# Kernel optimization log

Measured on AMD Instinct MI355X. Metric: run time of the kernel, lower is better.

The kernel has to match this reference:

```python
import jax, jax.numpy as jnp
import numpy as np

B, N, D = 1, 4096, 512
H, HD = 8, 64
NBINS = 512
CAND = 64
SCALE = 1.0 / np.sqrt(HD)
MAX_NORM = 1.0 - 1e-5
TWO_PI = 2.0 * np.pi


def _project(x):
    # Poincare-ball style projection: clip L2 norm of each point to MAX_NORM.
    n = jnp.sqrt(jnp.sum(x * x, axis=-1, keepdims=True))
    s = jnp.minimum(1.0, MAX_NORM / jnp.maximum(n, 1e-12))
    return x * s


def _bins(x):
    # Deterministic geometric binning (DavisCache stand-in): quantize the
    # angle of the first two coordinates into NBINS bins.
    ang = jnp.arctan2(x[..., 1], x[..., 0])  # (-pi, pi]
    b = jnp.floor((ang / TWO_PI + 0.5) * NBINS)
    return jnp.clip(b, 0, NBINS - 1).astype(jnp.int32)


def setup_inputs() -> dict:
    key0 = jax.random.key(0)
    ks = jax.random.split(key0, 12)
    w = 0.02  # typical init scale for projection weights
    return {
        "query": jax.random.normal(ks[0], (B, N, D), dtype=jnp.float32),
        "key": jax.random.normal(ks[1], (B, N, D), dtype=jnp.float32),
        "value": jax.random.normal(ks[2], (B, N, D), dtype=jnp.float32),
        "Wq": jax.random.normal(ks[3], (D, D), dtype=jnp.float32) * w,
        "bq": jnp.zeros((D,), dtype=jnp.float32),
        "Wk": jax.random.normal(ks[4], (D, D), dtype=jnp.float32) * w,
        "bk": jnp.zeros((D,), dtype=jnp.float32),
        "Wv": jax.random.normal(ks[5], (D, D), dtype=jnp.float32) * w,
        "bv": jnp.zeros((D,), dtype=jnp.float32),
        "Wo": jax.random.normal(ks[6], (D, D), dtype=jnp.float32) * w,
        "bo": jnp.zeros((D,), dtype=jnp.float32),
    }


def reference(query, key, value, Wq, bq, Wk, bk, Wv, bv, Wo, bo):
    Bq, Nq, Dm = query.shape
    Nk = key.shape[1]
    # projections + split heads -> (B, H, N, HD)
    q = (query @ Wq.T + bq).reshape(Bq, Nq, H, HD).transpose(0, 2, 1, 3)
    k = (key @ Wk.T + bk).reshape(Bq, Nk, H, HD).transpose(0, 2, 1, 3)
    v = (value @ Wv.T + bv).reshape(Bq, Nk, H, HD).transpose(0, 2, 1, 3)
    q = _project(q)
    k = _project(k)

    # geometric binning; candidate keys for a query are those whose bin is
    # within radius 1 of the query's bin (neighboring_bins, radius=1).
    qb = _bins(q)  # (B, H, Nq) int32
    kb = _bins(k)  # (B, H, Nk) int32
    mask = jnp.abs(qb[..., :, None] - kb[..., None, :]) <= 1  # (B,H,Nq,Nk)
    # fallback: if a query has no candidates, attend over all keys
    any_valid = jnp.any(mask, axis=-1, keepdims=True)
    eff = jnp.where(any_valid, mask, True)
    # keep only the first CAND candidates per query (by key index)
    rank = jnp.cumsum(eff.astype(jnp.int32), axis=-1) - 1
    sel = eff & (rank < CAND)

    scores = jnp.einsum("bhqd,bhkd->bhqk", q, k) * SCALE
    scores = jnp.where(sel, scores, -jnp.inf)
    attn = jax.nn.softmax(scores, axis=-1)  # dropout p=0.0 (eval mode)
    out = jnp.einsum("bhqk,bhkd->bhqd", attn, v)

    out = out.transpose(0, 2, 1, 3).reshape(Bq, Nq, Dm)
    return out @ Wo.T + bo
```

## Files before the change

kernel.cpp:

```cpp
#include <hip/hip_runtime.h>
#include <math.h>

typedef unsigned short u16;
typedef __attribute__((ext_vector_type(8))) short v8bf;
typedef __attribute__((ext_vector_type(4))) float f32x4;

#define N_TOK 4096
#define DMODEL 512
#define NHEAD 8
#define HDIM 64
#define CANDN 64
#define NBINS 512
#define BINCAP 64
#define QCAP 128
#define ATT_SCALE 0.125f
#define MAX_NORM_F 0.99999f

__device__ __forceinline__ float bf2f(u16 u) {
  union { unsigned int i; float f; } v; v.i = ((unsigned int)u) << 16; return v.f;
}
__device__ __forceinline__ u16 f2bf(float f) {
  union { float f; unsigned int i; } v; v.f = f;
  unsigned int x = v.i;
  return (u16)((x + 0x7fffu + ((x >> 16) & 1u)) >> 16);
}
__device__ __forceinline__ uint4 load_pack8(const float* __restrict__ p) {
  const float4 x0 = *(const float4*)p;
  const float4 x1 = *(const float4*)(p + 4);
  union { u16 h[8]; uint4 u; } r;
  r.h[0] = f2bf(x0.x); r.h[1] = f2bf(x0.y); r.h[2] = f2bf(x0.z); r.h[3] = f2bf(x0.w);
  r.h[4] = f2bf(x1.x); r.h[5] = f2bf(x1.y); r.h[6] = f2bf(x1.z); r.h[7] = f2bf(x1.w);
  return r.u;
}

__global__ __launch_bounds__(256) void prep_kernel(
    const float* __restrict__ query, const float* __restrict__ key_,
    const float* __restrict__ value,
    const float* __restrict__ Wq, const float* __restrict__ Wk,
    const float* __restrict__ Wv, const float* __restrict__ Wo,
    u16* __restrict__ qx, u16* __restrict__ kx, u16* __restrict__ vx,
    u16* __restrict__ wqx, u16* __restrict__ wkx, u16* __restrict__ wvx,
    u16* __restrict__ wox,
    int* __restrict__ qb, int* __restrict__ kb, unsigned char* __restrict__ flags,
    int* __restrict__ khist)
{
  __shared__ float xs[16 * 516];
  const int blk = blockIdx.x;
  const int tid = threadIdx.x;

  if (blk >= 4096) {
    int4 z4; z4.x = 0; z4.y = 0; z4.z = 0; z4.w = 0;
    ((int4*)khist)[((blk - 4096) << 8) + tid] = z4;
    return;
  }

  if (blk >= 512) {
    const int rel = blk - 512;
    const float* src; u16* dst; int base;
    if (rel < 1024)      { src = query; dst = qx; base = rel << 11; }
    else if (rel < 2048) { src = key_;  dst = kx; base = (rel - 1024) << 11; }
    else if (rel < 3072) { src = value; dst = vx; base = (rel - 2048) << 11; }
    else {
      const int r2 = rel - 3072; const int w = r2 >> 7;
      src = (w == 0) ? Wq : (w == 1) ? Wk : (w == 2) ? Wv : Wo;
      dst = (w == 0) ? wqx : (w == 1) ? wkx : (w == 2) ? wvx : wox;
      base = (r2 & 127) << 11;
    }
    const int off = base + tid * 8;
    *(uint4*)(dst + off) = load_pack8(src + off);
    return;
  }

  const int isk  = blk >> 8;
  const int tile = blk & 255;
  const float* X = isk ? key_ : query;
  const float* W = isk ? Wk : Wq;

#pragma unroll
  for (int i = 0; i < 8; ++i) {
    const int flat = i * 1024 + tid * 4;
    const int row = flat >> 9, col = flat & 511;
    *(float4*)&xs[row * 516 + col] = *(const float4*)(X + (tile * 16 + row) * DMODEL + col);
  }
  __syncthreads();

  const int n_local = tid >> 4;
  const int pair = tid & 15;
  const int h = pair >> 1, coord = pair & 1;
  const float* wrow = W + ((h << 6) + coord) * DMODEL;
  const float* xrow = &xs[n_local * 516];

  double c0 = 0.0, c1 = 0.0, c2 = 0.0, c3 = 0.0;
  for (int k = 0; k < DMODEL; k += 4) {
    const float4 xv = *(const float4*)(xrow + k);
    const float4 wv = *(const float4*)(wrow + k);
    c0 = fma((double)xv.x, (double)wv.x, c0);
    c1 = fma((double)xv.y, (double)wv.y, c1);
    c2 = fma((double)xv.z, (double)wv.z, c2);
    c3 = fma((double)xv.w, (double)wv.w, c3);
  }
  const double a = (c0 + c1) + (c2 + c3);
  const double other = __shfl_xor(a, 1);
  if (coord == 0) {
    const double a0 = a, a1 = other;
    const int n = tile * 16 + n_local;
    double ang = atan2(a1, a0);
    double t = (ang / 6.283185307179586 + 0.5) * 512.0;
    int b = (int)floor(t);
    b = b < 0 ? 0 : (b > 511 ? 511 : b);
    (isk ? kb : qb)[(h << 12) + n] = b;

    const double r = sqrt(a0 * a0 + a1 * a1);
    const double dist = fabs(t - nearbyint(t));
    const double margin = fmin(0.45, 3.3e-4 / fmax(r, 1e-30) + 5e-5);
    flags[(isk << 15) | (h << 12) | n] = (dist < margin) ? 1 : 0;
  }
}

__device__ float fdlibm_atanf(float x) {
#pragma clang fp contract(off)
  const float atanhi[4] = {4.6364760399e-01f, 7.8539812565e-01f,
                           9.8279368877e-01f, 1.5707962513e+00f};
  const float atanlo[4] = {5.0121582440e-09f, 3.7748947079e-08f,
                           3.4473217170e-08f, 7.5497894159e-08f};
  const float aT[5] = {3.3333328366e-01f, -1.9999158382e-01f, 1.4253635705e-01f,
                       -1.0648017377e-01f, 6.1687607318e-02f};
  unsigned ix = __float_as_uint(x);
  const unsigned sign = ix >> 31;
  ix &= 0x7fffffffu;
  int id;
  float z, w, s1, s2;
  if (ix >= 0x4c800000u) {
    z = atanhi[3] + 0x1p-120f;
    return sign ? -z : z;
  }
  if (ix < 0x3ee00000u) {
    if (ix < 0x39800000u) return x;
    id = -1;
  } else {
    x = fabsf(x);
    if (ix < 0x3f980000u) {
      if (ix < 0x3f300000u) { id = 0; x = (2.0f * x - 1.0f) / (2.0f + x); }
      else                  { id = 1; x = (x - 1.0f) / (x + 1.0f); }
    } else {
      if (ix < 0x401c0000u) { id = 2; x = (x - 1.5f) / (1.0f + 1.5f * x); }
      else                  { id = 3; x = -1.0f / x; }
    }
  }
  z = x * x;
  w = z * z;
  s1 = z * (aT[0] + w * (aT[2] + w * aT[4]));
  s2 = w * (aT[1] + w * aT[3]);
  if (id < 0) return x - x * (s1 + s2);
  z = atanhi[id] - ((x * (s1 + s2) - atanlo[id]) - x);
  return sign ? -z : z;
}

__device__ float fdlibm_atan2f(float y, float x) {
#pragma clang fp contract(off)
  const float pi = 3.1415927410e+00f, pi_lo = -8.7422776573e-08f;
  const unsigned hx = __float_as_uint(x), hy = __float_as_uint(y);
  if (hx == 0x3f800000u) return fdlibm_atanf(y);
  const unsigned m = ((hy >> 31) & 1u) | ((hx >> 30) & 2u);
  const unsigned ix = hx & 0x7fffffffu, iy = hy & 0x7fffffffu;
  if (iy == 0u) {
    switch (m) { case 0: case 1: return y; case 2: return pi; default: return -pi; }
  }
  if (ix == 0u) return (m & 1u) ? -1.57079637050628662f : 1.57079637050628662f;
  float z;
  if (ix + (26u << 23) < iy) {
    z = 1.57079637050628662f;
    return (m & 1u) ? -z : z;
  }
  if ((m & 2u) && iy + (26u << 23) < ix) z = 0.0f;
  else z = fdlibm_atanf(fabsf(y / x));
  switch (m) {
    case 0: return z;
    case 1: return -z;
    case 2: return pi - (z - pi_lo);
    default: return (z - pi_lo) - pi;
  }
}

__global__ __launch_bounds__(256) void gemmfix_kernel(
    const u16* __restrict__ qx, const u16* __restrict__ kx, const u16* __restrict__ vx,
    const u16* __restrict__ wqx, const u16* __restrict__ wkx, const u16* __restrict__ wvx,
    const float* __restrict__ bq, const float* __restrict__ bk, const float* __restrict__ bv,
    const float* __restrict__ query, const float* __restrict__ key_,
    const float* __restrict__ Wq, const float* __restrict__ Wk,
    const unsigned char* __restrict__ flags,
    int* __restrict__ qb, int* __restrict__ kb,
    u16* __restrict__ Qb, u16* __restrict__ Kb, u16* __restrict__ Vb)
{
  __shared__ u16 As[2][128 * 40];
  __shared__ u16 Ws[2][128 * 40];
  __shared__ int wle[64];
  __shared__ int wlc;

  const int blk = blockIdx.x;
  const int tid = threadIdx.x;

  if (blk >= 384) {
    const int slice = blk - 384;
    if (tid == 0) wlc = 0;
    __syncthreads();
    for (int i = tid; i < 1024; i += 256) {
      const int flat = slice * 1024 + i;
      if (flags[flat]) {
        const int p = atomicAdd(&wlc, 1);
        if (p < 64) wle[p] = flat;
      }
    }
    __syncthreads();
    int nw = wlc; if (nw > 64) nw = 64;
    const int w = tid >> 6, d = tid & 63;
    for (int e = w; e < nw; e += 4) {
      const int flat = wle[e];
      const int n = flat & 4095;
      const int h = (flat >> 12) & 7;
      const int isk = flat >> 15;
      const float* xr = (isk ? key_ : query) + n * DMODEL;
      const float* wr = (isk ? Wk : Wq) + ((h << 6) + d) * DMODEL;
      float acc = 0.0f;
      for (int k = 0; k < DMODEL; k += 16) {
        const float4 xa = *(const float4*)(xr + k);
        const float4 xb = *(const float4*)(xr + k + 4);
        const float4 xc = *(const float4*)(xr + k + 8);
        const float4 xd = *(const float4*)(xr + k + 12);
        const float4 wa = *(const float4*)(wr + k);
        const float4 wb = *(const float4*)(wr + k + 4);
        const float4 wc = *(const float4*)(wr + k + 8);
        const float4 wd = *(const float4*)(wr + k + 12);
        acc = __fmaf_rn(xa.x, wa.x, acc); acc = __fmaf_rn(xa.y, wa.y, acc);
        acc = __fmaf_rn(xa.z, wa.z, acc); acc = __fmaf_rn(xa.w, wa.w, acc);
        acc = __fmaf_rn(xb.x, wb.x, acc); acc = __fmaf_rn(xb.y, wb.y, acc);
        acc = __fmaf_rn(xb.z, wb.z, acc); acc = __fmaf_rn(xb.w, wb.w, acc);
        acc = __fmaf_rn(xc.x, wc.x, acc); acc = __fmaf_rn(xc.y, wc.y, acc);
        acc = __fmaf_rn(xc.z, wc.z, acc); acc = __fmaf_rn(xc.w, wc.w, acc);
        acc = __fmaf_rn(xd.x, wd.x, acc); acc = __fmaf_rn(xd.y, wd.y, acc);
        acc = __fmaf_rn(xd.z, wd.z, acc); acc = __fmaf_rn(xd.w, wd.w, acc);
      }
      {
#pragma clang fp contract(off)
        const float sq = acc * acc;
        float rr[8];
#pragma unroll
        for (int j = 0; j < 8; ++j) rr[j] = __shfl(sq, j);
        for (int i = 8; i < 64; i += 8) {
#pragma unroll
          for (int j = 0; j < 8; ++j) rr[j] += __shfl(sq, i + j);
        }
        const float ss = ((rr[0] + rr[1]) + (rr[2] + rr[3])) +
                         ((rr[4] + rr[5]) + (rr[6] + rr[7]));
        const float nrm = __fsqrt_rn(ss);
        const float s = fminf(1.0f, 0.99999f / fmaxf(nrm, 1e-12f));
        const float c0 = __shfl(acc, 0) * s;
        const float c1 = __shfl(acc, 1) * s;
        const float cr = (float)atan2((double)c1, (double)c0);
        const float fd = fdlibm_atan2f(c1, c0);
        const float tol = fmaxf(fabsf(cr) * 6e-7f, 1e-30f);
        const float ang = (fabsf(fd - cr) <= tol) ? fd : cr;
        const float t = ((ang / 6.2831854820251465f) + 0.5f) * 512.0f;
        int b = (int)floorf(t);
        b = b < 0 ? 0 : (b > 511 ? 511 : b);
        if (d == 0) (isk ? kb : qb)[(h << 12) + n] = b;
      }
    }
    return;
  }

  const int z = blk >> 7;
  const int rem = blk & 127;
  const int bm = (rem & 31) * 128;
  const int bn = (rem >> 5) * 128;

  const u16* A    = (z == 0) ? qx : (z == 1) ? kx : vx;
  const u16* W    = (z == 0) ? wqx : (z == 1) ? wkx : wvx;
  const float* bias = (z == 0) ? bq : (z == 1) ? bk : bv;
  u16* O          = (z == 0) ? Qb : (z == 1) ? Kb : Vb;

  const int lane = tid & 63;
  const int wave = tid >> 6;
  const int row4 = tid >> 2;
  const int seg  = tid & 3;
  const int wm = (wave & 1) * 64;
  const int wn = (wave >> 1) * 64;
  const int l15 = lane & 15;
  const int quad = lane >> 4;

  f32x4 acc[4][4] = {};

  uint4 a0 = *(const uint4*)(A + (bm + row4) * DMODEL + seg * 8);
  uint4 a1 = *(const uint4*)(A + (bm + row4 + 64) * DMODEL + seg * 8);
  uint4 w0 = *(const uint4*)(W + (bn + row4) * DMODEL + seg * 8);
  uint4 w1 = *(const uint4*)(W + (bn + row4 + 64) * DMODEL + seg * 8);

  for (int kt = 0; kt < DMODEL; kt += 32) {
    const int p = (kt >> 5) & 1;
    *(uint4*)&As[p][row4 * 40 + seg * 8] = a0;
    *(uint4*)&As[p][(row4 + 64) * 40 + seg * 8] = a1;
    *(uint4*)&Ws[p][row4 * 40 + seg * 8] = w0;
    *(uint4*)&Ws[p][(row4 + 64) * 40 + seg * 8] = w1;
    __syncthreads();
    if (kt + 32 < DMODEL) {
      a0 = *(const uint4*)(A + (bm + row4) * DMODEL + kt + 32 + seg * 8);
      a1 = *(const uint4*)(A + (bm + row4 + 64) * DMODEL + kt + 32 + seg * 8);
      w0 = *(const uint4*)(W + (bn + row4) * DMODEL + kt + 32 + seg * 8);
      w1 = *(const uint4*)(W + (bn + row4 + 64) * DMODEL + kt + 32 + seg * 8);
    }
    v8bf af[4], bfr[4];
#pragma unroll
    for (int i = 0; i < 4; ++i)
      af[i] = *(const v8bf*)&As[p][(wm + i * 16 + l15) * 40 + quad * 8];
#pragma unroll
    for (int j = 0; j < 4; ++j)
      bfr[j] = *(const v8bf*)&Ws[p][(wn + j * 16 + l15) * 40 + quad * 8];
#pragma unroll
    for (int i = 0; i < 4; ++i)
#pragma unroll
      for (int j = 0; j < 4; ++j)
        acc[i][j] = __builtin_amdgcn_mfma_f32_16x16x32_bf16(af[i], bfr[j], acc[i][j], 0, 0, 0);
  }

  float bval[4];
#pragma unroll
  for (int j = 0; j < 4; ++j) bval[j] = bias[bn + wn + j * 16 + l15];
  const int h = (bn + wn) >> 6;

#pragma unroll
  for (int i = 0; i < 4; ++i) {
#pragma unroll
    for (int r = 0; r < 4; ++r) {
      const int row = bm + wm + i * 16 + quad * 4 + r;
      float v0 = acc[i][0][r] + bval[0];
      float v1 = acc[i][1][r] + bval[1];
      float v2 = acc[i][2][r] + bval[2];
      float v3 = acc[i][3][r] + bval[3];
      if (z != 2) {
        float ss = v0 * v0 + v1 * v1 + v2 * v2 + v3 * v3;
#pragma unroll
        for (int o = 1; o < 16; o <<= 1) ss += __shfl_xor(ss, o);
        const float s = fminf(1.0f, MAX_NORM_F / fmaxf(sqrtf(ss), 1e-12f));
        v0 *= s; v1 *= s; v2 *= s; v3 *= s;
      }
      const int base = (((h << 12) + row) << 6) + l15;
      O[base +  0] = f2bf(v0); O[base + 16] = f2bf(v1);
      O[base + 32] = f2bf(v2); O[base + 48] = f2bf(v3);
    }
  }
}

__global__ __launch_bounds__(256) void bin_hist_kernel(
    const int* __restrict__ kb, const int* __restrict__ qb,
    int* __restrict__ khist, u16* __restrict__ blist,
    int* __restrict__ qhist, u16* __restrict__ qlist)
{
  const int h = blockIdx.x;
  const int type = blockIdx.y;
  const int* src = type ? qb : kb;
  int* hist = type ? qhist : khist;
  u16* list = type ? qlist : blist;
  const int cap = type ? QCAP : BINCAP;

  const int i = blockIdx.z * 256 + threadIdx.x;
  const int b = src[(h << 12) + i];
  const int pos = atomicAdd(&hist[(h << 9) + b], 1);
  if (pos < cap) list[((h << 9) + b) * cap + pos] = (u16)i;
}

__global__ __launch_bounds__(64) void attn_bin_kernel(
    const u16* __restrict__ Qb, const u16* __restrict__ Kb,
    const u16* __restrict__ Vb, const int* __restrict__ qhist,
    const u16* __restrict__ qlist, const int* __restrict__ khist,
    const u16* __restrict__ blist, u16* __restrict__ aout)
{
  __shared__ u16 kf[4 * 2 * 4 * 16 * 8];
  __shared__ u16 vf[4 * 2 * 4 * 16 * 8];
  __shared__ u16 pf[16 * 72];
  __shared__ u16 s_cand[64];
  __shared__ int s_qg[16];

  const int hb = blockIdx.x;
  const int h = hb >> 9;
  const int b = hb & 511;
  int qcnt = qhist[hb];
  if (qcnt > QCAP) qcnt = QCAP;
  if (qcnt == 0) return;

  const int lane = threadIdx.x;
  const int l15 = lane & 15;
  const int quad = lane >> 4;

  int v0 = 0xFFFF, v1 = 0xFFFF, v2 = 0xFFFF;
  int c0 = 0, c1 = 0, c2 = 0;
  if (b > 0) {
    c0 = khist[(h << 9) + b - 1];
    if (c0 > BINCAP) c0 = BINCAP;
    if (lane < c0) v0 = (int)blist[(((h << 9) + b - 1) << 6) + lane];
  }
  {
    c1 = khist[(h << 9) + b];
    if (c1 > BINCAP) c1 = BINCAP;
    if (lane < c1) v1 = (int)blist[(((h << 9) + b) << 6) + lane];
  }
  if (b < NBINS - 1) {
    c2 = khist[(h << 9) + b + 1];
    if (c2 > BINCAP) c2 = BINCAP;
    if (lane < c2) v2 = (int)blist[(((h << 9) + b + 1) << 6) + lane];
  }

  int r0 = 0, r1 = 0, r2 = 0;
#pragma unroll 8
  for (int j = 0; j < 64; ++j) {
    const int w0 = __shfl(v0, j);
    const int w1 = __shfl(v1, j);
    const int w2 = __shfl(v2, j);
    r0 += (w0 < v0) + (w1 < v0) + (w2 < v0);
    r1 += (w0 < v1) + (w1 < v1) + (w2 < v1);
    r2 += (w0 < v2) + (w1 < v2) + (w2 < v2);
  }
  const int tot = c0 + c1 + c2;
  const int ccnt = tot < CANDN ? tot : CANDN;
  const int ccnt_eff = (tot == 0) ? 64 : ccnt;
  if (tot == 0) {
    s_cand[lane] = (u16)lane;
  } else {
    if (v0 != 0xFFFF && r0 < CANDN) s_cand[r0] = (u16)v0;
    if (v1 != 0xFFFF && r1 < CANDN) s_cand[r1] = (u16)v1;
    if (v2 != 0xFFFF && r2 < CANDN) s_cand[r2] = (u16)v2;
  }
  __syncthreads();
  if (tot > 0 && lane >= ccnt) s_cand[lane] = s_cand[0];
  __syncthreads();

  {
    const int r = lane >> 3, s = lane & 7;
    const int ks = s >> 2, qd = s & 3;
#pragma unroll
    for (int it = 0; it < 8; ++it) {
      const int key = it * 8 + r;
      const int c = s_cand[key];
      const uint4 kv = *(const uint4*)(Kb + ((h << 18) | (c << 6)) + s * 8);
      const int idx = ((((key >> 4) * 2 + ks) * 4 + qd) * 16 + (key & 15)) * 8;
      *(uint4*)&kf[idx] = kv;
    }
  }
  {
    const int r = lane >> 3, s = lane & 7;
    const int nt = s >> 1, d0 = (s & 1) * 8;
#pragma unroll
    for (int it = 0; it < 8; ++it) {
      const int key = it * 8 + r;
      const int c = s_cand[key];
      union { u16 hh[8]; uint4 u; } vv;
      vv.u = *(const uint4*)(Vb + ((h << 18) | (c << 6)) + s * 8);
      const int kstep = key >> 5, qd = (key >> 3) & 3, j = key & 7;
#pragma unroll
      for (int m = 0; m < 8; ++m)
        vf[(((nt * 2 + kstep) * 4 + qd) * 16 + d0 + m) * 8 + j] = vv.hh[m];
    }
  }
  __syncthreads();

  v8bf akf[4][2], bvf[4][2];
#pragma unroll
  for (int t = 0; t < 4; ++t)
#pragma unroll
    for (int ks = 0; ks < 2; ++ks) {
      akf[t][ks] = *(const v8bf*)&kf[(((t * 2 + ks) * 4 + quad) * 16 + l15) * 8];
      bvf[t][ks] = *(const v8bf*)&vf[(((t * 2 + ks) * 4 + quad) * 16 + l15) * 8];
    }

  const int nchunk = (qcnt + 15) >> 4;
  for (int ci = 0; ci < nchunk; ++ci) {
    const int base = ci << 4;
    const int qcn = min(16, qcnt - base);
    __syncthreads();
    if (lane < 16) {
      int idx = base + lane;
      if (idx > qcnt - 1) idx = qcnt - 1;
      s_qg[lane] = (int)qlist[(hb << 7) + idx];
    }
    __syncthreads();

    const u16* qrow = Qb + ((h << 18) | (s_qg[l15] << 6));
    v8bf bq[2];
#pragma unroll
    for (int ks = 0; ks < 2; ++ks)
      bq[ks] = *(const v8bf*)(qrow + ks * 32 + quad * 8);

    float sc[16];
    __builtin_amdgcn_s_setprio(1);
#pragma unroll
    for (int t = 0; t < 4; ++t) {
      f32x4 sa = {0.f, 0.f, 0.f, 0.f};
      sa = __builtin_amdgcn_mfma_f32_16x16x32_bf16(akf[t][0], bq[0], sa, 0, 0, 0);
      sa = __builtin_amdgcn_mfma_f32_16x16x32_bf16(akf[t][1], bq[1], sa, 0, 0, 0);
#pragma unroll
      for (int r = 0; r < 4; ++r) {
        const int key = t * 16 + quad * 4 + r;
        sc[t * 4 + r] = (key < ccnt_eff) ? sa[r] * ATT_SCALE : -INFINITY;
      }
    }
    __builtin_amdgcn_s_setprio(0);
    float mx = sc[0];
#pragma unroll
    for (int i = 1; i < 16; ++i) mx = fmaxf(mx, sc[i]);
    mx = fmaxf(mx, __shfl_xor(mx, 16));
    mx = fmaxf(mx, __shfl_xor(mx, 32));
    float sum = 0.0f;
    float pe[16];
#pragma unroll
    for (int i = 0; i < 16; ++i) { pe[i] = __expf(sc[i] - mx); sum += pe[i]; }
    sum += __shfl_xor(sum, 16);
    sum += __shfl_xor(sum, 32);
    const float inv = 1.0f / sum;

    __syncthreads();
#pragma unroll
    for (int t = 0; t < 4; ++t)
#pragma unroll
      for (int r = 0; r < 4; ++r)
        pf[l15 * 72 + t * 16 + quad * 4 + r] = f2bf(pe[t * 4 + r] * inv);
    __syncthreads();

    v8bf ap[2];
#pragma unroll
    for (int ks = 0; ks < 2; ++ks)
      ap[ks] = *(const v8bf*)&pf[l15 * 72 + ks * 32 + quad * 8];

    __builtin_amdgcn_s_setprio(1);
#pragma unroll
    for (int nt = 0; nt < 4; ++nt) {
      f32x4 o = {0.f, 0.f, 0.f, 0.f};
      o = __builtin_amdgcn_mfma_f32_16x16x32_bf16(ap[0], bvf[nt][0], o, 0, 0, 0);
      o = __builtin_amdgcn_mfma_f32_16x16x32_bf16(ap[1], bvf[nt][1], o, 0, 0, 0);
#pragma unroll
      for (int r = 0; r < 4; ++r) {
        const int row = quad * 4 + r;
        if (row < qcn)
          aout[s_qg[row] * DMODEL + (h << 6) + nt * 16 + l15] = f2bf(o[r]);
      }
    }
    __builtin_amdgcn_s_setprio(0);
  }
}

__global__ __launch_bounds__(256) void gemm_out_kernel(
    const u16* __restrict__ A, const u16* __restrict__ W,
    const float* __restrict__ bias, float* __restrict__ O)
{
  __shared__ u16 As[2][128 * 40];
  __shared__ u16 Ws[2][128 * 40];

  const int tid  = threadIdx.x;
  const int lane = tid & 63;
  const int wave = tid >> 6;
  const int row4 = tid >> 2;
  const int seg  = tid & 3;

  const int bm = blockIdx.x * 128;
  const int bn = blockIdx.y * 128;
  const int wm = (wave & 1) * 64;
  const int wn = (wave >> 1) * 64;
  const int l15 = lane & 15;
  const int quad = lane >> 4;

  f32x4 acc[4][4] = {};

  uint4 a0 = *(const uint4*)(A + (bm + row4) * DMODEL + seg * 8);
  uint4 a1 = *(const uint4*)(A + (bm + row4 + 64) * DMODEL + seg * 8);
  uint4 w0 = *(const uint4*)(W + (bn + row4) * DMODEL + seg * 8);
  uint4 w1 = *(const uint4*)(W + (bn + row4 + 64) * DMODEL + seg * 8);

  for (int kt = 0; kt < DMODEL; kt += 32) {
    const int p = (kt >> 5) & 1;
    *(uint4*)&As[p][row4 * 40 + seg * 8] = a0;
    *(uint4*)&As[p][(row4 + 64) * 40 + seg * 8] = a1;
    *(uint4*)&Ws[p][row4 * 40 + seg * 8] = w0;
    *(uint4*)&Ws[p][(row4 + 64) * 40 + seg * 8] = w1;
    __syncthreads();
    if (kt + 32 < DMODEL) {
      a0 = *(const uint4*)(A + (bm + row4) * DMODEL + kt + 32 + seg * 8);
      a1 = *(const uint4*)(A + (bm + row4 + 64) * DMODEL + kt + 32 + seg * 8);
      w0 = *(const uint4*)(W + (bn + row4) * DMODEL + kt + 32 + seg * 8);
      w1 = *(const uint4*)(W + (bn + row4 + 64) * DMODEL + kt + 32 + seg * 8);
    }
    v8bf af[4], bfr[4];
#pragma unroll
    for (int i = 0; i < 4; ++i)
      af[i] = *(const v8bf*)&As[p][(wm + i * 16 + l15) * 40 + quad * 8];
#pragma unroll
    for (int j = 0; j < 4; ++j)
      bfr[j] = *(const v8bf*)&Ws[p][(wn + j * 16 + l15) * 40 + quad * 8];
#pragma unroll
    for (int i = 0; i < 4; ++i)
#pragma unroll
      for (int j = 0; j < 4; ++j)
        acc[i][j] = __builtin_amdgcn_mfma_f32_16x16x32_bf16(af[i], bfr[j], acc[i][j], 0, 0, 0);
  }

#pragma unroll
  for (int j = 0; j < 4; ++j) {
    const int cg = bn + wn + j * 16 + l15;
    const float bval = bias[cg];
#pragma unroll
    for (int i = 0; i < 4; ++i) {
      const int rbase = bm + wm + i * 16 + quad * 4;
#pragma unroll
      for (int r = 0; r < 4; ++r)
        O[(rbase + r) * DMODEL + cg] = acc[i][j][r] + bval;
    }
  }
}

extern "C" void kernel_launch(void* const* d_in, const int* in_sizes, int n_in,
                              void* d_out, int out_size, void* d_ws, size_t ws_size,
                              hipStream_t stream) {
  const float* query = (const float*)d_in[0];
  const float* key_  = (const float*)d_in[1];
  const float* value = (const float*)d_in[2];
  const float* Wq = (const float*)d_in[3];
  const float* bq = (const float*)d_in[4];
  const float* Wk = (const float*)d_in[5];
  const float* bk = (const float*)d_in[6];
  const float* Wv = (const float*)d_in[7];
  const float* bv = (const float*)d_in[8];
  const float* Wo = (const float*)d_in[9];
  const float* bo = (const float*)d_in[10];

  char* ws = (char*)d_ws;
  u16* qx    = (u16*)(ws);
  u16* kx    = (u16*)(ws + 4194304);
  u16* vx    = (u16*)(ws + 8388608);
  u16* wqx   = (u16*)(ws + 12582912);
  u16* wkx   = (u16*)(ws + 13107200);
  u16* wvx   = (u16*)(ws + 13631488);
  u16* wox   = (u16*)(ws + 14155776);
  u16* Qb    = (u16*)(ws + 14680064);
  u16* Kb    = (u16*)(ws + 18874368);
  u16* Vb    = (u16*)(ws + 23068672);
  u16* aout  = (u16*)(ws + 27262976);
  int* qb    = (int*)(ws + 31457280);
  int* kb    = (int*)(ws + 31588352);
  unsigned char* flags = (unsigned char*)(ws + 31719424);
  int* khist = (int*)(ws + 31784960);
  int* qhist = (int*)(ws + 31801344);
  u16* blist = (u16*)(ws + 31817728);
  u16* qlist = (u16*)(ws + 32342016);

  prep_kernel<<<4104, 256, 0, stream>>>(
      query, key_, value, Wq, Wk, Wv, Wo,
      qx, kx, vx, wqx, wkx, wvx, wox, qb, kb, flags, khist);
  gemmfix_kernel<<<448, 256, 0, stream>>>(
      qx, kx, vx, wqx, wkx, wvx, bq, bk, bv,
      query, key_, Wq, Wk, flags, qb, kb, Qb, Kb, Vb);
  bin_hist_kernel<<<dim3(8, 2, 16), 256, 0, stream>>>(
      kb, qb, khist, blist, qhist, qlist);
  attn_bin_kernel<<<4096, 64, 0, stream>>>(
      Qb, Kb, Vb, qhist, qlist, khist, blist, aout);
  gemm_out_kernel<<<dim3(32, 4), 256, 0, stream>>>(aout, wox, bo, (float*)d_out);
}
```

Baseline: 213.1 us.

## Split bin-fix into own kernel, grid-stride prep conversion, halve output GEMM M-tile

The prep kernel's conversion and histogram-zeroing blocks become one grid-stride loop over fewer blocks. The fp32 bin-fix work moves out of the QKV GEMM kernel into a separate kernel with 512 smaller slices, so the fix work no longer tails behind the GEMM blocks. The output GEMM tile shrinks from 128 to 64 rows, doubling its grid to fill more CUs. This adds one more kernel launch and lowers per-block reuse in the output GEMM.

After: 200.3 us. 6.0% less time.

```diff
diff --git a/kernel.cpp b/kernel.cpp
--- a/kernel.cpp
+++ b/kernel.cpp
@@ -48,26 +48,27 @@
   const int blk = blockIdx.x;
   const int tid = threadIdx.x;
 
-  if (blk >= 4096) {
-    int4 z4; z4.x = 0; z4.y = 0; z4.z = 0; z4.w = 0;
-    ((int4*)khist)[((blk - 4096) << 8) + tid] = z4;
-    return;
-  }
-
   if (blk >= 512) {
-    const int rel = blk - 512;
-    const float* src; u16* dst; int base;
-    if (rel < 1024)      { src = query; dst = qx; base = rel << 11; }
-    else if (rel < 2048) { src = key_;  dst = kx; base = (rel - 1024) << 11; }
-    else if (rel < 3072) { src = value; dst = vx; base = (rel - 2048) << 11; }
-    else {
-      const int r2 = rel - 3072; const int w = r2 >> 7;
-      src = (w == 0) ? Wq : (w == 1) ? Wk : (w == 2) ? Wv : Wo;
-      dst = (w == 0) ? wqx : (w == 1) ? wkx : (w == 2) ? wvx : wox;
-      base = (r2 & 127) << 11;
-    }
-    const int off = base + tid * 8;
-    *(uint4*)(dst + off) = load_pack8(src + off);
+    const int base = ((blk - 512) << 8) + tid;
+    for (int u = base; u < 919552; u += 262144) {
+      if (u < 786432) {
+        const int third = u >> 18;
+        const int off = (u & 262143) << 3;
+        const float* src = (third == 0) ? query : (third == 1) ? key_ : value;
+        u16* dst = (third == 0) ? qx : (third == 1) ? kx : vx;
+        *(uint4*)(dst + off) = load_pack8(src + off);
+      } else if (u < 917504) {
+        const int r2 = u - 786432;
+        const int w = r2 >> 15;
+        const int off = (r2 & 32767) << 3;
+        const float* src = (w == 0) ? Wq : (w == 1) ? Wk : (w == 2) ? Wv : Wo;
+        u16* dst = (w == 0) ? wqx : (w == 1) ? wkx : (w == 2) ? wvx : wox;
+        *(uint4*)(dst + off) = load_pack8(src + off);
+      } else {
+        int4 z4; z4.x = 0; z4.y = 0; z4.z = 0; z4.w = 0;
+        ((int4*)khist)[u - 917504] = z4;
+      }
+    }
     return;
   }
 
@@ -182,92 +183,95 @@
   }
 }
 
-__global__ __launch_bounds__(256) void gemmfix_kernel(
+__global__ __launch_bounds__(256) void binfix_kernel(
+    const float* __restrict__ query, const float* __restrict__ key_,
+    const float* __restrict__ Wq, const float* __restrict__ Wk,
+    const unsigned char* __restrict__ flags,
+    int* __restrict__ qb, int* __restrict__ kb)
+{
+  __shared__ int wle[64];
+  __shared__ int wlc;
+
+  const int tid = threadIdx.x;
+  const int slice = blockIdx.x;
+
+  if (tid == 0) wlc = 0;
+  __syncthreads();
+  if (tid < 128) {
+    const int flat = (slice << 7) + tid;
+    if (flags[flat]) {
+      const int p = atomicAdd(&wlc, 1);
+      if (p < 64) wle[p] = flat;
+    }
+  }
+  __syncthreads();
+  int nw = wlc; if (nw > 64) nw = 64;
+  const int w = tid >> 6, d = tid & 63;
+  for (int e = w; e < nw; e += 4) {
+    const int flat = wle[e];
+    const int n = flat & 4095;
+    const int h = (flat >> 12) & 7;
+    const int isk = flat >> 15;
+    const float* xr = (isk ? key_ : query) + n * DMODEL;
+    const float* wr = (isk ? Wk : Wq) + ((h << 6) + d) * DMODEL;
+    float acc = 0.0f;
+    for (int k = 0; k < DMODEL; k += 16) {
+      const float4 xa = *(const float4*)(xr + k);
+      const float4 xb = *(const float4*)(xr + k + 4);
+      const float4 xc = *(const float4*)(xr + k + 8);
+      const float4 xd = *(const float4*)(xr + k + 12);
+      const float4 wa = *(const float4*)(wr + k);
+      const float4 wb = *(const float4*)(wr + k + 4);
+      const float4 wc = *(const float4*)(wr + k + 8);
+      const float4 wd = *(const float4*)(wr + k + 12);
+      acc = __fmaf_rn(xa.x, wa.x, acc); acc = __fmaf_rn(xa.y, wa.y, acc);
+      acc = __fmaf_rn(xa.z, wa.z, acc); acc = __fmaf_rn(xa.w, wa.w, acc);
+      acc = __fmaf_rn(xb.x, wb.x, acc); acc = __fmaf_rn(xb.y, wb.y, acc);
+      acc = __fmaf_rn(xb.z, wb.z, acc); acc = __fmaf_rn(xb.w, wb.w, acc);
+      acc = __fmaf_rn(xc.x, wc.x, acc); acc = __fmaf_rn(xc.y, wc.y, acc);
+      acc = __fmaf_rn(xc.z, wc.z, acc); acc = __fmaf_rn(xc.w, wc.w, acc);
+      acc = __fmaf_rn(xd.x, wd.x, acc); acc = __fmaf_rn(xd.y, wd.y, acc);
+      acc = __fmaf_rn(xd.z, wd.z, acc); acc = __fmaf_rn(xd.w, wd.w, acc);
+    }
+    {
+#pragma clang fp contract(off)
+      const float sq = acc * acc;
+      float rr[8];
+#pragma unroll
+      for (int j = 0; j < 8; ++j) rr[j] = __shfl(sq, j);
+      for (int i = 8; i < 64; i += 8) {
+#pragma unroll
+        for (int j = 0; j < 8; ++j) rr[j] += __shfl(sq, i + j);
+      }
+      const float ss = ((rr[0] + rr[1]) + (rr[2] + rr[3])) +
+                       ((rr[4] + rr[5]) + (rr[6] + rr[7]));
+      const float nrm = __fsqrt_rn(ss);
+      const float s = fminf(1.0f, 0.99999f / fmaxf(nrm, 1e-12f));
+      const float c0 = __shfl(acc, 0) * s;
+      const float c1 = __shfl(acc, 1) * s;
+      const float cr = (float)atan2((double)c1, (double)c0);
+      const float fd = fdlibm_atan2f(c1, c0);
+      const float tol = fmaxf(fabsf(cr) * 6e-7f, 1e-30f);
+      const float ang = (fabsf(fd - cr) <= tol) ? fd : cr;
+      const float t = ((ang / 6.2831854820251465f) + 0.5f) * 512.0f;
+      int b = (int)floorf(t);
+      b = b < 0 ? 0 : (b > 511 ? 511 : b);
+      if (d == 0) (isk ? kb : qb)[(h << 12) + n] = b;
+    }
+  }
+}
+
+__global__ __launch_bounds__(256) void gemm_qkv_kernel(
     const u16* __restrict__ qx, const u16* __restrict__ kx, const u16* __restrict__ vx,
     const u16* __restrict__ wqx, const u16* __restrict__ wkx, const u16* __restrict__ wvx,
     const float* __restrict__ bq, const float* __restrict__ bk, const float* __restrict__ bv,
-    const float* __restrict__ query, const float* __restrict__ key_,
-    const float* __restrict__ Wq, const float* __restrict__ Wk,
-    const unsigned char* __restrict__ flags,
-    int* __restrict__ qb, int* __restrict__ kb,
     u16* __restrict__ Qb, u16* __restrict__ Kb, u16* __restrict__ Vb)
 {
   __shared__ u16 As[2][128 * 40];
   __shared__ u16 Ws[2][128 * 40];
-  __shared__ int wle[64];
-  __shared__ int wlc;
 
   const int blk = blockIdx.x;
   const int tid = threadIdx.x;
-
-  if (blk >= 384) {
-    const int slice = blk - 384;
-    if (tid == 0) wlc = 0;
-    __syncthreads();
-    for (int i = tid; i < 1024; i += 256) {
-      const int flat = slice * 1024 + i;
-      if (flags[flat]) {
-        const int p = atomicAdd(&wlc, 1);
-        if (p < 64) wle[p] = flat;
-      }
-    }
-    __syncthreads();
-    int nw = wlc; if (nw > 64) nw = 64;
-    const int w = tid >> 6, d = tid & 63;
-    for (int e = w; e < nw; e += 4) {
-      const int flat = wle[e];
-      const int n = flat & 4095;
-      const int h = (flat >> 12) & 7;
-      const int isk = flat >> 15;
-      const float* xr = (isk ? key_ : query) + n * DMODEL;
-      const float* wr = (isk ? Wk : Wq) + ((h << 6) + d) * DMODEL;
-      float acc = 0.0f;
-      for (int k = 0; k < DMODEL; k += 16) {
-        const float4 xa = *(const float4*)(xr + k);
-        const float4 xb = *(const float4*)(xr + k + 4);
-        const float4 xc = *(const float4*)(xr + k + 8);
-        const float4 xd = *(const float4*)(xr + k + 12);
-        const float4 wa = *(const float4*)(wr + k);
-        const float4 wb = *(const float4*)(wr + k + 4);
-        const float4 wc = *(const float4*)(wr + k + 8);
-        const float4 wd = *(const float4*)(wr + k + 12);
-        acc = __fmaf_rn(xa.x, wa.x, acc); acc = __fmaf_rn(xa.y, wa.y, acc);
-        acc = __fmaf_rn(xa.z, wa.z, acc); acc = __fmaf_rn(xa.w, wa.w, acc);
-        acc = __fmaf_rn(xb.x, wb.x, acc); acc = __fmaf_rn(xb.y, wb.y, acc);
-        acc = __fmaf_rn(xb.z, wb.z, acc); acc = __fmaf_rn(xb.w, wb.w, acc);
-        acc = __fmaf_rn(xc.x, wc.x, acc); acc = __fmaf_rn(xc.y, wc.y, acc);
-        acc = __fmaf_rn(xc.z, wc.z, acc); acc = __fmaf_rn(xc.w, wc.w, acc);
-        acc = __fmaf_rn(xd.x, wd.x, acc); acc = __fmaf_rn(xd.y, wd.y, acc);
-        acc = __fmaf_rn(xd.z, wd.z, acc); acc = __fmaf_rn(xd.w, wd.w, acc);
-      }
-      {
-#pragma clang fp contract(off)
-        const float sq = acc * acc;
-        float rr[8];
-#pragma unroll
-        for (int j = 0; j < 8; ++j) rr[j] = __shfl(sq, j);
-        for (int i = 8; i < 64; i += 8) {
-#pragma unroll
-          for (int j = 0; j < 8; ++j) rr[j] += __shfl(sq, i + j);
-        }
-        const float ss = ((rr[0] + rr[1]) + (rr[2] + rr[3])) +
-                         ((rr[4] + rr[5]) + (rr[6] + rr[7]));
-        const float nrm = __fsqrt_rn(ss);
-        const float s = fminf(1.0f, 0.99999f / fmaxf(nrm, 1e-12f));
-        const float c0 = __shfl(acc, 0) * s;
-        const float c1 = __shfl(acc, 1) * s;
-        const float cr = (float)atan2((double)c1, (double)c0);
-        const float fd = fdlibm_atan2f(c1, c0);
-        const float tol = fmaxf(fabsf(cr) * 6e-7f, 1e-30f);
-        const float ang = (fabsf(fd - cr) <= tol) ? fd : cr;
-        const float t = ((ang / 6.2831854820251465f) + 0.5f) * 512.0f;
-        int b = (int)floorf(t);
-        b = b < 0 ? 0 : (b > 511 ? 511 : b);
-        if (d == 0) (isk ? kb : qb)[(h << 12) + n] = b;
-      }
-    }
-    return;
-  }
 
   const int z = blk >> 7;
   const int rem = blk & 127;
@@ -550,7 +554,7 @@
     const u16* __restrict__ A, const u16* __restrict__ W,
     const float* __restrict__ bias, float* __restrict__ O)
 {
-  __shared__ u16 As[2][128 * 40];
+  __shared__ u16 As[2][64 * 40];
   __shared__ u16 Ws[2][128 * 40];
 
   const int tid  = threadIdx.x;
@@ -559,42 +563,39 @@
   const int row4 = tid >> 2;
   const int seg  = tid & 3;
 
-  const int bm = blockIdx.x * 128;
+  const int bm = blockIdx.x * 64;
   const int bn = blockIdx.y * 128;
-  const int wm = (wave & 1) * 64;
+  const int wm = (wave & 1) * 32;
   const int wn = (wave >> 1) * 64;
   const int l15 = lane & 15;
   const int quad = lane >> 4;
 
-  f32x4 acc[4][4] = {};
+  f32x4 acc[2][4] = {};
 
   uint4 a0 = *(const uint4*)(A + (bm + row4) * DMODEL + seg * 8);
-  uint4 a1 = *(const uint4*)(A + (bm + row4 + 64) * DMODEL + seg * 8);
   uint4 w0 = *(const uint4*)(W + (bn + row4) * DMODEL + seg * 8);
   uint4 w1 = *(const uint4*)(W + (bn + row4 + 64) * DMODEL + seg * 8);
 
   for (int kt = 0; kt < DMODEL; kt += 32) {
     const int p = (kt >> 5) & 1;
     *(uint4*)&As[p][row4 * 40 + seg * 8] = a0;
-    *(uint4*)&As[p][(row4 + 64) * 40 + seg * 8] = a1;
     *(uint4*)&Ws[p][row4 * 40 + seg * 8] = w0;
     *(uint4*)&Ws[p][(row4 + 64) * 40 + seg * 8] = w1;
     __syncthreads();
     if (kt + 32 < DMODEL) {
       a0 = *(const uint4*)(A + (bm + row4) * DMODEL + kt + 32 + seg * 8);
-      a1 = *(const uint4*)(A + (bm + row4 + 64) * DMODEL + kt + 32 + seg * 8);
       w0 = *(const uint4*)(W + (bn + row4) * DMODEL + kt + 32 + seg * 8);
       w1 = *(const uint4*)(W + (bn + row4 + 64) * DMODEL + kt + 32 + seg * 8);
     }
-    v8bf af[4], bfr[4];
-#pragma unroll
-    for (int i = 0; i < 4; ++i)
+    v8bf af[2], bfr[4];
+#pragma unroll
+    for (int i = 0; i < 2; ++i)
       af[i] = *(const v8bf*)&As[p][(wm + i * 16 + l15) * 40 + quad * 8];
 #pragma unroll
     for (int j = 0; j < 4; ++j)
       bfr[j] = *(const v8bf*)&Ws[p][(wn + j * 16 + l15) * 40 + quad * 8];
 #pragma unroll
-    for (int i = 0; i < 4; ++i)
+    for (int i = 0; i < 2; ++i)
 #pragma unroll
       for (int j = 0; j < 4; ++j)
         acc[i][j] = __builtin_amdgcn_mfma_f32_16x16x32_bf16(af[i], bfr[j], acc[i][j], 0, 0, 0);
@@ -605,7 +606,7 @@
     const int cg = bn + wn + j * 16 + l15;
     const float bval = bias[cg];
 #pragma unroll
-    for (int i = 0; i < 4; ++i) {
+    for (int i = 0; i < 2; ++i) {
       const int rbase = bm + wm + i * 16 + quad * 4;
 #pragma unroll
       for (int r = 0; r < 4; ++r)
@@ -649,15 +650,16 @@
   u16* blist = (u16*)(ws + 31817728);
   u16* qlist = (u16*)(ws + 32342016);
 
-  prep_kernel<<<4104, 256, 0, stream>>>(
+  prep_kernel<<<1536, 256, 0, stream>>>(
       query, key_, value, Wq, Wk, Wv, Wo,
       qx, kx, vx, wqx, wkx, wvx, wox, qb, kb, flags, khist);
-  gemmfix_kernel<<<448, 256, 0, stream>>>(
-      qx, kx, vx, wqx, wkx, wvx, bq, bk, bv,
-      query, key_, Wq, Wk, flags, qb, kb, Qb, Kb, Vb);
+  binfix_kernel<<<512, 256, 0, stream>>>(
+      query, key_, Wq, Wk, flags, qb, kb);
+  gemm_qkv_kernel<<<384, 256, 0, stream>>>(
+      qx, kx, vx, wqx, wkx, wvx, bq, bk, bv, Qb, Kb, Vb);
   bin_hist_kernel<<<dim3(8, 2, 16), 256, 0, stream>>>(
       kb, qb, khist, blist, qhist, qlist);
   attn_bin_kernel<<<4096, 64, 0, stream>>>(
       Qb, Kb, Vb, qhist, qlist, khist, blist, aout);
-  gemm_out_kernel<<<dim3(32, 4), 256, 0, stream>>>(aout, wox, bo, (float*)d_out);
-}
+  gemm_out_kernel<<<dim3(64, 4), 256, 0, stream>>>(aout, wox, bo, (float*)d_out);
+}
```
